# Kernel tuning notes

Hardware: AMD Instinct MI355X
Metric: run time of the kernel (lower is better)

The kernel has to match this reference:

```python
import jax, jax.numpy as jnp
import numpy as np

B = 32; H = 56; W = 56; C = 192; WS = 7; SHIFT = 3; NH = 6
HD = C // NH; N = WS * WS; MLP = 4 * C; NWH = H // WS; NWW = W // WS
EPS = 1e-5


def _rel_pos_index():
    coords = np.stack(np.meshgrid(np.arange(WS), np.arange(WS), indexing='ij'))  # (2,WS,WS)
    cf = coords.reshape(2, -1)                      # (2, N)
    rel = (cf[:, :, None] - cf[:, None, :]).transpose(1, 2, 0).astype(np.int64)  # (N,N,2)
    rel[..., 0] += WS - 1
    rel[..., 1] += WS - 1
    rel[..., 0] *= 2 * WS - 1
    return jnp.asarray(rel.sum(-1))                 # (N, N) int

REL_IDX = _rel_pos_index()


def _shift_mask():
    img = np.zeros((1, H, W, 1), np.float32)
    cnt = 0
    for hs in (slice(0, -WS), slice(-WS, -SHIFT), slice(-SHIFT, None)):
        for ws_ in (slice(0, -WS), slice(-WS, -SHIFT), slice(-SHIFT, None)):
            img[:, hs, ws_, :] = cnt
            cnt += 1
    mw = img.reshape(1, NWH, WS, NWW, WS, 1).transpose(0, 1, 3, 2, 4, 5).reshape(-1, N)
    am = mw[:, None, :] - mw[:, :, None]
    return jnp.asarray(np.where(am != 0, -100.0, 0.0).astype(np.float32))  # (nW, N, N)


def setup_inputs() -> dict:
    key = jax.random.key(0)
    ks = jax.random.split(key, 8)
    s = 0.02
    return {
        'x': jax.random.normal(ks[0], (B, H * W, C), jnp.float32),
        'attn_mask': _shift_mask(),
        'norm1_w': jnp.ones((C,), jnp.float32),
        'norm1_b': jnp.zeros((C,), jnp.float32),
        'qkv_w': jax.random.normal(ks[1], (3 * C, C), jnp.float32) * s,
        'qkv_b': jnp.zeros((3 * C,), jnp.float32),
        'rpb_table': jax.random.normal(ks[2], ((2 * WS - 1) ** 2, NH), jnp.float32) * s,
        'proj_w': jax.random.normal(ks[3], (C, C), jnp.float32) * s,
        'proj_b': jnp.zeros((C,), jnp.float32),
        'norm2_w': jnp.ones((C,), jnp.float32),
        'norm2_b': jnp.zeros((C,), jnp.float32),
        'fc1_w': jax.random.normal(ks[4], (MLP, C), jnp.float32) * s,
        'fc1_b': jnp.zeros((MLP,), jnp.float32),
        'fc2_w': jax.random.normal(ks[5], (C, MLP), jnp.float32) * s,
        'fc2_b': jnp.zeros((C,), jnp.float32),
    }


def _ln(x, w, b):
    m = jnp.mean(x, axis=-1, keepdims=True)
    v = jnp.mean(jnp.square(x - m), axis=-1, keepdims=True)
    return (x - m) * jax.lax.rsqrt(v + EPS) * w + b


def reference(x, attn_mask, norm1_w, norm1_b, qkv_w, qkv_b, rpb_table,
              proj_w, proj_b, norm2_w, norm2_b, fc1_w, fc1_b, fc2_w, fc2_b):
    shortcut = x
    xs = _ln(x, norm1_w, norm1_b).reshape(B, H, W, C)
    # cyclic shift
    xs = jnp.roll(xs, (-SHIFT, -SHIFT), axis=(1, 2))
    # window partition -> (B*nW, N, C)
    xw = xs.reshape(B, NWH, WS, NWW, WS, C).transpose(0, 1, 3, 2, 4, 5).reshape(-1, N, C)
    B_ = xw.shape[0]
    # qkv
    qkv = xw @ qkv_w.T + qkv_b                       # (B_, N, 3C)
    qkv = qkv.reshape(B_, N, 3, NH, HD).transpose(2, 0, 3, 1, 4)
    q, k, v = qkv[0], qkv[1], qkv[2]                 # (B_, NH, N, HD)
    scale = HD ** -0.5
    attn = jnp.einsum('bhnd,bhmd->bhnm', q * scale, k)
    # relative position bias: (N,N,NH) -> (NH,N,N)
    bias = rpb_table[REL_IDX.reshape(-1)].reshape(N, N, NH).transpose(2, 0, 1)
    attn = attn + bias[None]
    # shift mask: (nW, N, N)
    nW = attn_mask.shape[0]
    attn = attn.reshape(B_ // nW, nW, NH, N, N) + attn_mask[None, :, None]
    attn = jax.nn.softmax(attn.reshape(B_, NH, N, N), axis=-1)
    out = jnp.einsum('bhnm,bhmd->bhnd', attn, v)     # (B_, NH, N, HD)
    out = out.transpose(0, 2, 1, 3).reshape(B_, N, C)
    out = out @ proj_w.T + proj_b
    # window reverse -> (B, H, W, C)
    xr = out.reshape(B, NWH, NWW, WS, WS, C).transpose(0, 1, 3, 2, 4, 5).reshape(B, H, W, C)
    xr = jnp.roll(xr, (SHIFT, SHIFT), axis=(1, 2)).reshape(B, H * W, C)
    x = shortcut + xr
    # MLP
    h = _ln(x, norm2_w, norm2_b)
    h = jax.nn.gelu(h @ fc1_w.T + fc1_b, approximate=False)
    h = h @ fc2_w.T + fc2_b
    return x + h
```

## Files before the change

### kernel.cpp

```cpp
#include <hip/hip_runtime.h>
#include <hip/hip_bf16.h>

typedef unsigned short u16;
typedef __attribute__((ext_vector_type(8))) short bf16x8;
typedef __attribute__((ext_vector_type(4))) float f32x4;

#define MFMA16(a, b, c) __builtin_amdgcn_mfma_f32_16x16x32_bf16(a, b, c, 0, 0, 0)

__device__ __forceinline__ u16 f2b(float f) {
  union { float f; unsigned u; } x; x.f = f;
  return (u16)((x.u + 0x7fffu + ((x.u >> 16) & 1u)) >> 16);
}

__device__ __forceinline__ void gload_lds16(const void* g, void* l) {
  __builtin_amdgcn_global_load_lds(
      (const __attribute__((address_space(1))) void*)g,
      (__attribute__((address_space(3))) void*)l, 16, 0, 0);
}

template <int NCH>
__device__ __forceinline__ void stage_frags(const u16* __restrict__ src,
                                            u16* dst, int wave, int lane) {
#pragma unroll
  for (int it = 0; it < NCH / 4; ++it) {
    int chunk = it * 4 + wave;
    gload_lds16(src + ((size_t)chunk * 64 + lane) * 8, dst + chunk * 512);
  }
}

__global__ __launch_bounds__(256) void pack_kernel(const float* __restrict__ W,
                                                   u16* __restrict__ F, int NT,
                                                   int KS, int K, int kmajor) {
  int f = blockIdx.x * 256 + threadIdx.x;
  if (f >= NT * KS * 64) return;
  int l = f & 63, rest = f >> 6;
  int ks, ct;
  if (kmajor) { ct = rest % NT; ks = rest / NT; }
  else        { ks = rest % KS; ct = rest / KS; }
  int row = ct * 16 + (l & 15);
  int col = ks * 32 + (l >> 4) * 8;
  const float* s = W + (size_t)row * K + col;
  u16* d = F + (size_t)f * 8;
#pragma unroll
  for (int i = 0; i < 8; ++i) d[i] = f2b(s[i]);
}

__global__ __launch_bounds__(256) void pack2_kernel(const float* __restrict__ W,
                                                    u16* __restrict__ F) {
  int f = blockIdx.x * 256 + threadIdx.x;
  if (f >= 24 * 12 * 64) return;
  int l = f & 63, rest = f >> 6;
  int ct = rest % 12, hs = rest / 12;
  int row = ct * 16 + (l & 15);
  int g = l >> 4;
  u16* d = F + (size_t)f * 8;
#pragma unroll
  for (int i = 0; i < 8; ++i) {
    int h = hs * 32 + (i < 4 ? 4 * g + i : 16 + 4 * g + (i - 4));
    d[i] = f2b(W[(size_t)row * 768 + h]);
  }
}

__global__ __launch_bounds__(256) void pack_proj_pi(const float* __restrict__ W,
                                                    u16* __restrict__ F) {
  int f = blockIdx.x * 256 + threadIdx.x;
  if (f >= 72 * 64) return;
  int l = f & 63, rest = f >> 6;
  int half = rest / 36, r2 = rest - half * 36;
  int ks = r2 / 6, ctl = r2 - ks * 6;
  int row = (half * 6 + ctl) * 16 + (l & 15);
  int g = l >> 4;
  u16* d = F + (size_t)f * 8;
#pragma unroll
  for (int i = 0; i < 8; ++i) {
    int k = ks * 32 + (i < 4 ? 4 * g + i : 16 + 4 * g + (i - 4));
    d[i] = f2b(W[(size_t)row * 192 + k]);
  }
}

__global__ __launch_bounds__(256, 3) void attn_win(
    const float* __restrict__ x, const float* __restrict__ n1w,
    const float* __restrict__ n1b, const u16* __restrict__ qkvwf,
    const float* __restrict__ qkvb_, const float* __restrict__ rpb,
    const float* __restrict__ amask, const u16* __restrict__ pwf,
    const float* __restrict__ pb, float* __restrict__ out) {
  __shared__ __align__(16) u16 lds[25088];
  u16* wbuf = lds;
  u16* sA   = lds;
  u16* klds = lds + 18432;
  u16* vlds = lds + 21000;
  int tid = threadIdx.x, wave = tid >> 6, lane = tid & 63;
  int g = lane >> 4, c = lane & 15, wr = wave * 16;
  int wing = blockIdx.x;
  int wi = wing & 63;
  {
    float vals[12][4];
    int srcrow[4];
#pragma unroll
    for (int reg = 0; reg < 4; ++reg) {
      int n = wr + 4 * g + reg;
      if (n > 48) n = 48;
      int bb = wing >> 6, wloc = wing & 63, wh = wloc >> 3, ww = wloc & 7;
      int rr = n / 7, cc = n - rr * 7;
      int hs = wh * 7 + rr + 3; if (hs >= 56) hs -= 56;
      int wsr = ww * 7 + cc + 3; if (wsr >= 56) wsr -= 56;
      srcrow[reg] = bb * 3136 + hs * 56 + wsr;
    }
#pragma unroll
    for (int nt = 0; nt < 12; ++nt)
#pragma unroll
      for (int reg = 0; reg < 4; ++reg)
        vals[nt][reg] = x[(size_t)srcrow[reg] * 192 + nt * 16 + c];
#pragma unroll
    for (int reg = 0; reg < 4; ++reg) {
      float s = 0.f;
#pragma unroll
      for (int nt = 0; nt < 12; ++nt) s += vals[nt][reg];
      s += __shfl_xor(s, 1, 64); s += __shfl_xor(s, 2, 64);
      s += __shfl_xor(s, 4, 64); s += __shfl_xor(s, 8, 64);
      float m = s * (1.f / 192.f), q = 0.f;
#pragma unroll
      for (int nt = 0; nt < 12; ++nt) { float d = vals[nt][reg] - m; q += d * d; }
      q += __shfl_xor(q, 1, 64); q += __shfl_xor(q, 2, 64);
      q += __shfl_xor(q, 4, 64); q += __shfl_xor(q, 8, 64);
      float rs = rsqrtf(q * (1.f / 192.f) + 1e-5f);
#pragma unroll
      for (int nt = 0; nt < 12; ++nt) vals[nt][reg] = (vals[nt][reg] - m) * rs;
    }
#pragma unroll
    for (int nt = 0; nt < 12; ++nt) {
      float wv = n1w[nt * 16 + c], bv = n1b[nt * 16 + c];
#pragma unroll
      for (int reg = 0; reg < 4; ++reg) {
        int r = wr + 4 * g + reg;
        int ch = nt * 2 + (c >> 3);
        int ph = (ch & 24) | ((ch ^ (r & 7)) & 7);
        sA[r * 192 + ph * 8 + (c & 7)] = f2b(vals[nt][reg] * wv + bv);
      }
    }
  }
  __syncthreads();
  bf16x8 afr[6];
  {
    int ar = wr + c;
#pragma unroll
    for (int ks = 0; ks < 6; ++ks) {
      int ch = ks * 4 + g;
      int ph = (ch & 24) | ((ch ^ (ar & 7)) & 7);
      afr[ks] = *(const bf16x8*)(sA + ar * 192 + ph * 8);
    }
  }
  __syncthreads();
#pragma unroll
  for (int s = 0; s < 3; ++s)
    stage_frags<12>(qkvwf + (size_t)((s * 12 + 0) * 6) * 512, wbuf + s * 6144,
                    wave, lane);
  int nq = wr + c;
  int nb = nq > 48 ? 48 : nq;
  int ridx[16];
  float pm[16];
  {
    int i1 = nb / 7, j1 = nb - i1 * 7;
#pragma unroll
    for (int kt = 0; kt < 4; ++kt)
#pragma unroll
      for (int reg = 0; reg < 4; ++reg) {
        int m = kt * 16 + 4 * g + reg;
        int idx = kt * 4 + reg;
        if (m < 49) {
          int i2 = m / 7, j2 = m - i2 * 7;
          ridx[idx] = ((i1 - i2 + 6) * 13 + (j1 - j2 + 6)) * 6;
          pm[idx] = amask[(size_t)wi * 2401 + nb * 49 + m];
        } else {
          ridx[idx] = 0;
          pm[idx] = -1e30f;
        }
      }
  }
  __syncthreads();
  bf16x8 ofr[6];
#pragma unroll
  for (int h = 0; h < 6; ++h) {
    f32x4 qa[2], ka[2], va[2];
#pragma unroll
    for (int s = 0; s < 3; ++s)
#pragma unroll
      for (int t = 0; t < 2; ++t) {
        f32x4 acc = {0.f, 0.f, 0.f, 0.f};
#pragma unroll
        for (int ks = 0; ks < 6; ++ks) {
          bf16x8 wf = *(const bf16x8*)(wbuf + (s * 12 + t * 6 + ks) * 512 +
                                       lane * 8);
          acc = MFMA16(wf, afr[ks], acc);
        }
        float4 b4 = *(const float4*)(qkvb_ + s * 192 + h * 32 + t * 16 + 4 * g);
#pragma unroll
        for (int reg = 0; reg < 4; ++reg) acc[reg] += ((const float*)&b4)[reg];
        if (s == 0) qa[t] = acc;
        else if (s == 1) ka[t] = acc;
        else va[t] = acc;
      }
    union { u16 hh[8]; bf16x8 v; } qf, kf;
#pragma unroll
    for (int reg = 0; reg < 4; ++reg) {
      qf.hh[reg] = f2b(qa[0][reg]);
      qf.hh[reg + 4] = f2b(qa[1][reg]);
      kf.hh[reg] = f2b(ka[0][reg]);
      kf.hh[reg + 4] = f2b(ka[1][reg]);
    }
    *(bf16x8*)(klds + nq * 40 + g * 8) = kf.v;
#pragma unroll
    for (int t = 0; t < 2; ++t)
#pragma unroll
      for (int reg = 0; reg < 4; ++reg)
        vlds[(t * 16 + 4 * g + reg) * 68 + nq] = f2b(va[t][reg]);
    __syncthreads();
    if (h < 5) {
#pragma unroll
      for (int s = 0; s < 3; ++s)
        stage_frags<12>(qkvwf + (size_t)((s * 12 + (h + 1) * 2) * 6) * 512,
                        wbuf + s * 6144, wave, lane);
    }
    float sv[16];
#pragma unroll
    for (int kt = 0; kt < 4; ++kt) {
      bf16x8 kw = *(const bf16x8*)(klds + (kt * 16 + c) * 40 + g * 8);
      f32x4 z = {0.f, 0.f, 0.f, 0.f};
      f32x4 sacc = MFMA16(kw, qf.v, z);
#pragma unroll
      for (int reg = 0; reg < 4; ++reg) sv[kt * 4 + reg] = sacc[reg];
    }
    const float scale = 0.17677669529663687f;
    float mx = -1e30f;
#pragma unroll
    for (int i = 0; i < 16; ++i) {
      sv[i] = sv[i] * scale + rpb[ridx[i] + h] + pm[i];
      mx = fmaxf(mx, sv[i]);
    }
    mx = fmaxf(mx, __shfl_xor(mx, 16, 64));
    mx = fmaxf(mx, __shfl_xor(mx, 32, 64));
    float se = 0.f;
#pragma unroll
    for (int i = 0; i < 16; ++i) {
      sv[i] = __expf(sv[i] - mx);
      se += sv[i];
    }
    se += __shfl_xor(se, 16, 64);
    se += __shfl_xor(se, 32, 64);
    float inv = 1.0f / se;
    union { u16 hh[8]; bf16x8 v; } pu0, pu1;
#pragma unroll
    for (int reg = 0; reg < 4; ++reg) {
      pu0.hh[reg] = f2b(sv[0 * 4 + reg] * inv);
      pu0.hh[reg + 4] = f2b(sv[1 * 4 + reg] * inv);
      pu1.hh[reg] = f2b(sv[2 * 4 + reg] * inv);
      pu1.hh[reg + 4] = f2b(sv[3 * 4 + reg] * inv);
    }
    f32x4 oacc[2] = {{0, 0, 0, 0}, {0, 0, 0, 0}};
#pragma unroll
    for (int nt = 0; nt < 2; ++nt)
#pragma unroll
      for (int mblk = 0; mblk < 2; ++mblk) {
        const u16* vp = vlds + (nt * 16 + c) * 68 + mblk * 32 + 4 * g;
        union { u16 hh[8]; bf16x8 v; } vt;
        *(short4*)(vt.hh) = *(const short4*)(vp);
        *(short4*)(vt.hh + 4) = *(const short4*)(vp + 16);
        oacc[nt] = MFMA16(vt.v, mblk ? pu1.v : pu0.v, oacc[nt]);
      }
    {
      union { u16 hh[8]; bf16x8 v; } of_;
#pragma unroll
      for (int reg = 0; reg < 4; ++reg) {
        of_.hh[reg] = f2b(oacc[0][reg]);
        of_.hh[reg + 4] = f2b(oacc[1][reg]);
      }
      ofr[h] = of_.v;
    }
    __syncthreads();
  }
  size_t trow = 0;
  if (nq < 49) {
    int rr = nq / 7, cc2 = nq - rr * 7;
    int wloc = wing & 63, wh = wloc >> 3, ww2 = wloc & 7;
    int hs2 = wh * 7 + rr + 3; if (hs2 >= 56) hs2 -= 56;
    int ws2 = ww2 * 7 + cc2 + 3; if (ws2 >= 56) ws2 -= 56;
    trow = (size_t)(wing >> 6) * 3136 + hs2 * 56 + ws2;
  }
#pragma unroll
  for (int half = 0; half < 2; ++half) {
#pragma unroll
    for (int it = 0; it < 9; ++it) {
      int chunk = it * 4 + wave;
      gload_lds16(pwf + ((size_t)(half * 36 + chunk) * 64 + lane) * 8,
                  lds + chunk * 512);
    }
    asm volatile("s_waitcnt vmcnt(0)" ::: "memory");
    __syncthreads();
    f32x4 op6[6];
#pragma unroll
    for (int i = 0; i < 6; ++i) op6[i] = (f32x4){0.f, 0.f, 0.f, 0.f};
#pragma unroll
    for (int ks = 0; ks < 6; ++ks)
#pragma unroll
      for (int ctl = 0; ctl < 6; ++ctl) {
        bf16x8 wf = *(const bf16x8*)(lds + (ks * 6 + ctl) * 512 + lane * 8);
        op6[ctl] = MFMA16(wf, ofr[ks], op6[ctl]);
      }
    if (nq < 49) {
      float* rowp = out + trow * 192 + half * 96;
      const float* xp = x + trow * 192 + half * 96;
#pragma unroll
      for (int ctl = 0; ctl < 6; ++ctl) {
        int colo = ctl * 16 + 4 * g;
        float4 xv = *(const float4*)(xp + colo);
        float4 b4 = *(const float4*)(pb + half * 96 + colo);
        float4 st;
        st.x = xv.x + op6[ctl][0] + b4.x;
        st.y = xv.y + op6[ctl][1] + b4.y;
        st.z = xv.z + op6[ctl][2] + b4.z;
        st.w = xv.w + op6[ctl][3] + b4.w;
        *(float4*)(rowp + colo) = st;
      }
    }
    __syncthreads();
  }
}

__global__ __launch_bounds__(256, 3) void mlp_fused(
    const float* __restrict__ n2w, const float* __restrict__ n2b,
    const u16* __restrict__ w1f, const float* __restrict__ b1,
    const u16* __restrict__ w2f, const float* __restrict__ b2,
    float* __restrict__ out) {
  __shared__ __align__(16) u16 lds[24576];
  u16* c1a = lds;
  u16* c1b = lds + 6144;
  u16* c2a = lds + 12288;
  u16* c2b = lds + 18432;
  u16* sA  = lds;
  int tid = threadIdx.x, wave = tid >> 6, lane = tid & 63;
  int g = lane >> 4, c = lane & 15, wr = wave * 16;
  int m0 = blockIdx.x * 64;
  {
    float v[12][4];
    int rr[4];
#pragma unroll
    for (int reg = 0; reg < 4; ++reg) rr[reg] = m0 + wr + 4 * g + reg;
#pragma unroll
    for (int nt = 0; nt < 12; ++nt)
#pragma unroll
      for (int reg = 0; reg < 4; ++reg)
        v[nt][reg] = out[(size_t)rr[reg] * 192 + nt * 16 + c];
#pragma unroll
    for (int reg = 0; reg < 4; ++reg) {
      float s = 0.f;
#pragma unroll
      for (int nt = 0; nt < 12; ++nt) s += v[nt][reg];
      s += __shfl_xor(s, 1, 64); s += __shfl_xor(s, 2, 64);
      s += __shfl_xor(s, 4, 64); s += __shfl_xor(s, 8, 64);
      float m = s * (1.f / 192.f), q = 0.f;
#pragma unroll
      for (int nt = 0; nt < 12; ++nt) { float d = v[nt][reg] - m; q += d * d; }
      q += __shfl_xor(q, 1, 64); q += __shfl_xor(q, 2, 64);
      q += __shfl_xor(q, 4, 64); q += __shfl_xor(q, 8, 64);
      float rs = rsqrtf(q * (1.f / 192.f) + 1e-5f);
#pragma unroll
      for (int nt = 0; nt < 12; ++nt) v[nt][reg] = (v[nt][reg] - m) * rs;
    }
#pragma unroll
    for (int nt = 0; nt < 12; ++nt) {
      float wv = n2w[nt * 16 + c], bv = n2b[nt * 16 + c];
#pragma unroll
      for (int reg = 0; reg < 4; ++reg) {
        int r = wr + 4 * g + reg;
        int ch = nt * 2 + (c >> 3);
        int ph = (ch & 24) | ((ch ^ (r & 7)) & 7);
        sA[r * 192 + ph * 8 + (c & 7)] = f2b(v[nt][reg] * wv + bv);
      }
    }
  }
  __syncthreads();
  bf16x8 afr[6];
  {
    int ar = wr + c;
#pragma unroll
    for (int ks = 0; ks < 6; ++ks) {
      int ch = ks * 4 + g;
      int ph = (ch & 24) | ((ch ^ (ar & 7)) & 7);
      afr[ks] = *(const bf16x8*)(sA + ar * 192 + ph * 8);
    }
  }
  __syncthreads();
  stage_frags<12>(w1f, c1a, wave, lane);
  stage_frags<12>(w2f, c2a, wave, lane);
  f32x4 o[12];
#pragma unroll
  for (int i = 0; i < 12; ++i) o[i] = (f32x4){0.f, 0.f, 0.f, 0.f};
  __syncthreads();
  for (int j = 0; j < 24; ++j) {
    int cur = j & 1;
    const u16* r1 = cur ? c1b : c1a;
    const u16* r2 = cur ? c2b : c2a;
    if (j < 23) {
      stage_frags<12>(w1f + (size_t)(j + 1) * 6144, cur ? c1a : c1b, wave, lane);
      stage_frags<12>(w2f + (size_t)(j + 1) * 6144, cur ? c2a : c2b, wave, lane);
    }
    f32x4 S1[2] = {{0,0,0,0},{0,0,0,0}};
#pragma unroll
    for (int ks = 0; ks < 6; ++ks) {
      bf16x8 w0 = *(const bf16x8*)(r1 + (0 * 6 + ks) * 512 + lane * 8);
      bf16x8 w1v = *(const bf16x8*)(r1 + (1 * 6 + ks) * 512 + lane * 8);
      S1[0] = MFMA16(w0, afr[ks], S1[0]);
      S1[1] = MFMA16(w1v, afr[ks], S1[1]);
    }
    union { u16 h[8]; bf16x8 v; } pu;
    float4 bv0 = *(const float4*)(b1 + j * 32 + 4 * g);
    float4 bv1 = *(const float4*)(b1 + j * 32 + 16 + 4 * g);
#pragma unroll
    for (int r = 0; r < 4; ++r) {
      float v0 = S1[0][r] + ((const float*)&bv0)[r];
      float u20 = v0 * (1.5957691216f + 0.0713548163f * v0 * v0);
      pu.h[r] = f2b(v0 / (1.f + __expf(-u20)));
      float v1 = S1[1][r] + ((const float*)&bv1)[r];
      float u21 = v1 * (1.5957691216f + 0.0713548163f * v1 * v1);
      pu.h[r + 4] = f2b(v1 / (1.f + __expf(-u21)));
    }
#pragma unroll
    for (int ct = 0; ct < 12; ++ct) {
      bf16x8 wf2 = *(const bf16x8*)(r2 + ct * 512 + lane * 8);
      o[ct] = MFMA16(wf2, pu.v, o[ct]);
    }
    __syncthreads();
  }
  size_t rowoff = (size_t)(m0 + wr + c) * 192;
#pragma unroll
  for (int ct = 0; ct < 12; ++ct) {
    float4 b4 = *(const float4*)(b2 + ct * 16 + 4 * g);
#pragma unroll
    for (int r = 0; r < 4; ++r) {
      size_t oo = rowoff + ct * 16 + 4 * g + r;
      out[oo] = out[oo] + o[ct][r] + ((const float*)&b4)[r];
    }
  }
}

extern "C" void kernel_launch(void* const* d_in, const int* in_sizes, int n_in,
                              void* d_out, int out_size, void* d_ws, size_t ws_size,
                              hipStream_t stream) {
  (void)in_sizes; (void)n_in; (void)out_size; (void)ws_size;
  const float* x     = (const float*)d_in[0];
  const float* amask = (const float*)d_in[1];
  const float* n1w   = (const float*)d_in[2];
  const float* n1b   = (const float*)d_in[3];
  const float* qkvw  = (const float*)d_in[4];
  const float* qkvb  = (const float*)d_in[5];
  const float* rpb   = (const float*)d_in[6];
  const float* projw = (const float*)d_in[7];
  const float* projb = (const float*)d_in[8];
  const float* n2w   = (const float*)d_in[9];
  const float* n2b   = (const float*)d_in[10];
  const float* fc1w  = (const float*)d_in[11];
  const float* fc1b  = (const float*)d_in[12];
  const float* fc2w  = (const float*)d_in[13];
  const float* fc2b  = (const float*)d_in[14];
  float* out = (float*)d_out;
  char* ws = (char*)d_ws;

  u16* qkvwf = (u16*)(ws);
  u16* projwf = (u16*)(ws + 221184);
  u16* fc1wf = (u16*)(ws + 221184 + 73728);
  u16* fc2wf = (u16*)(ws + 221184 + 73728 + 294912);

  pack_kernel<<<(36 * 6 * 64 + 255) / 256, 256, 0, stream>>>(qkvw, qkvwf, 36, 6, 192, 0);
  pack_proj_pi<<<(72 * 64 + 255) / 256, 256, 0, stream>>>(projw, projwf);
  pack_kernel<<<(48 * 6 * 64 + 255) / 256, 256, 0, stream>>>(fc1w, fc1wf, 48, 6, 192, 0);
  pack2_kernel<<<(24 * 12 * 64 + 255) / 256, 256, 0, stream>>>(fc2w, fc2wf);

  attn_win<<<2048, 256, 0, stream>>>(x, n1w, n1b, qkvwf, qkvb, rpb, amask,
                                     projwf, projb, out);

  mlp_fused<<<1568, 256, 0, stream>>>(n2w, n2b, fc1wf, fc1b, fc2wf, fc2b,
                                      out);
}
```

Measured before the change: 254.5 us.

## Single-buffer MLP weights for higher occupancy, prefetch proj weights, use native bf16 cvt

The MLP kernel drops double-buffered weight staging, which halves its LDS and raises launch bounds to 6 blocks per CU, but each step now waits synchronously for the next weight load. The attention kernel starts loading the first half of the projection weights during the last head iteration and trims its LDS allocation. Manual bf16 rounding is replaced with the HIP intrinsic conversion, and divisions become hardware reciprocals. Together these aim to raise occupancy and cut ALU work, at the cost of losing load/compute overlap in the MLP loop.

Result: slower. 449.4 us (+76.6%).

```diff
diff --git a/kernel.cpp b/kernel.cpp
--- a/kernel.cpp
+++ b/kernel.cpp
@@ -10,6 +10,12 @@
 __device__ __forceinline__ u16 f2b(float f) {
   union { float f; unsigned u; } x; x.f = f;
   return (u16)((x.u + 0x7fffu + ((x.u >> 16) & 1u)) >> 16);
+}
+
+__device__ __forceinline__ u16 f2bn(float f) {
+  union { __hip_bfloat16 b; u16 u; } cv;
+  cv.b = __float2bfloat16(f);
+  return cv.u;
 }
 
 __device__ __forceinline__ void gload_lds16(const void* g, void* l) {
@@ -84,7 +90,7 @@
     const float* __restrict__ qkvb_, const float* __restrict__ rpb,
     const float* __restrict__ amask, const u16* __restrict__ pwf,
     const float* __restrict__ pb, float* __restrict__ out) {
-  __shared__ __align__(16) u16 lds[25088];
+  __shared__ __align__(16) u16 lds[23176];
   u16* wbuf = lds;
   u16* sA   = lds;
   u16* klds = lds + 18432;
@@ -135,7 +141,7 @@
         int r = wr + 4 * g + reg;
         int ch = nt * 2 + (c >> 3);
         int ph = (ch & 24) | ((ch ^ (r & 7)) & 7);
-        sA[r * 192 + ph * 8 + (c & 7)] = f2b(vals[nt][reg] * wv + bv);
+        sA[r * 192 + ph * 8 + (c & 7)] = f2bn(vals[nt][reg] * wv + bv);
       }
     }
   }
@@ -203,23 +209,25 @@
     union { u16 hh[8]; bf16x8 v; } qf, kf;
 #pragma unroll
     for (int reg = 0; reg < 4; ++reg) {
-      qf.hh[reg] = f2b(qa[0][reg]);
-      qf.hh[reg + 4] = f2b(qa[1][reg]);
-      kf.hh[reg] = f2b(ka[0][reg]);
-      kf.hh[reg + 4] = f2b(ka[1][reg]);
+      qf.hh[reg] = f2bn(qa[0][reg]);
+      qf.hh[reg + 4] = f2bn(qa[1][reg]);
+      kf.hh[reg] = f2bn(ka[0][reg]);
+      kf.hh[reg + 4] = f2bn(ka[1][reg]);
     }
     *(bf16x8*)(klds + nq * 40 + g * 8) = kf.v;
 #pragma unroll
     for (int t = 0; t < 2; ++t)
 #pragma unroll
       for (int reg = 0; reg < 4; ++reg)
-        vlds[(t * 16 + 4 * g + reg) * 68 + nq] = f2b(va[t][reg]);
+        vlds[(t * 16 + 4 * g + reg) * 68 + nq] = f2bn(va[t][reg]);
     __syncthreads();
     if (h < 5) {
 #pragma unroll
       for (int s = 0; s < 3; ++s)
         stage_frags<12>(qkvwf + (size_t)((s * 12 + (h + 1) * 2) * 6) * 512,
                         wbuf + s * 6144, wave, lane);
+    } else {
+      stage_frags<36>(pwf, wbuf, wave, lane);
     }
     float sv[16];
 #pragma unroll
@@ -247,14 +255,14 @@
     }
     se += __shfl_xor(se, 16, 64);
     se += __shfl_xor(se, 32, 64);
-    float inv = 1.0f / se;
+    float inv = __builtin_amdgcn_rcpf(se);
     union { u16 hh[8]; bf16x8 v; } pu0, pu1;
 #pragma unroll
     for (int reg = 0; reg < 4; ++reg) {
-      pu0.hh[reg] = f2b(sv[0 * 4 + reg] * inv);
-      pu0.hh[reg + 4] = f2b(sv[1 * 4 + reg] * inv);
-      pu1.hh[reg] = f2b(sv[2 * 4 + reg] * inv);
-      pu1.hh[reg + 4] = f2b(sv[3 * 4 + reg] * inv);
+      pu0.hh[reg] = f2bn(sv[0 * 4 + reg] * inv);
+      pu0.hh[reg + 4] = f2bn(sv[1 * 4 + reg] * inv);
+      pu1.hh[reg] = f2bn(sv[2 * 4 + reg] * inv);
+      pu1.hh[reg + 4] = f2bn(sv[3 * 4 + reg] * inv);
     }
     f32x4 oacc[2] = {{0, 0, 0, 0}, {0, 0, 0, 0}};
 #pragma unroll
@@ -271,8 +279,8 @@
       union { u16 hh[8]; bf16x8 v; } of_;
 #pragma unroll
       for (int reg = 0; reg < 4; ++reg) {
-        of_.hh[reg] = f2b(oacc[0][reg]);
-        of_.hh[reg + 4] = f2b(oacc[1][reg]);
+        of_.hh[reg] = f2bn(oacc[0][reg]);
+        of_.hh[reg + 4] = f2bn(oacc[1][reg]);
       }
       ofr[h] = of_.v;
     }
@@ -288,14 +296,6 @@
   }
 #pragma unroll
   for (int half = 0; half < 2; ++half) {
-#pragma unroll
-    for (int it = 0; it < 9; ++it) {
-      int chunk = it * 4 + wave;
-      gload_lds16(pwf + ((size_t)(half * 36 + chunk) * 64 + lane) * 8,
-                  lds + chunk * 512);
-    }
-    asm volatile("s_waitcnt vmcnt(0)" ::: "memory");
-    __syncthreads();
     f32x4 op6[6];
 #pragma unroll
     for (int i = 0; i < 6; ++i) op6[i] = (f32x4){0.f, 0.f, 0.f, 0.f};
@@ -322,21 +322,23 @@
         *(float4*)(rowp + colo) = st;
       }
     }
-    __syncthreads();
-  }
-}
-
-__global__ __launch_bounds__(256, 3) void mlp_fused(
+    if (half == 0) {
+      __syncthreads();
+      stage_frags<36>(pwf + (size_t)36 * 512, lds, wave, lane);
+      __syncthreads();
+    }
+  }
+}
+
+__global__ __launch_bounds__(256, 6) void mlp_fused(
     const float* __restrict__ n2w, const float* __restrict__ n2b,
     const u16* __restrict__ w1f, const float* __restrict__ b1,
     const u16* __restrict__ w2f, const float* __restrict__ b2,
     float* __restrict__ out) {
-  __shared__ __align__(16) u16 lds[24576];
-  u16* c1a = lds;
-  u16* c1b = lds + 6144;
-  u16* c2a = lds + 12288;
-  u16* c2b = lds + 18432;
-  u16* sA  = lds;
+  __shared__ __align__(16) u16 lds[12288];
+  u16* c1 = lds;
+  u16* c2 = lds + 6144;
+  u16* sA = lds;
   int tid = threadIdx.x, wave = tid >> 6, lane = tid & 63;
   int g = lane >> 4, c = lane & 15, wr = wave * 16;
   int m0 = blockIdx.x * 64;
@@ -374,7 +376,7 @@
         int r = wr + 4 * g + reg;
         int ch = nt * 2 + (c >> 3);
         int ph = (ch & 24) | ((ch ^ (r & 7)) & 7);
-        sA[r * 192 + ph * 8 + (c & 7)] = f2b(v[nt][reg] * wv + bv);
+        sA[r * 192 + ph * 8 + (c & 7)] = f2bn(v[nt][reg] * wv + bv);
       }
     }
   }
@@ -390,25 +392,18 @@
     }
   }
   __syncthreads();
-  stage_frags<12>(w1f, c1a, wave, lane);
-  stage_frags<12>(w2f, c2a, wave, lane);
+  stage_frags<12>(w1f, c1, wave, lane);
+  stage_frags<12>(w2f, c2, wave, lane);
   f32x4 o[12];
 #pragma unroll
   for (int i = 0; i < 12; ++i) o[i] = (f32x4){0.f, 0.f, 0.f, 0.f};
   __syncthreads();
   for (int j = 0; j < 24; ++j) {
-    int cur = j & 1;
-    const u16* r1 = cur ? c1b : c1a;
-    const u16* r2 = cur ? c2b : c2a;
-    if (j < 23) {
-      stage_frags<12>(w1f + (size_t)(j + 1) * 6144, cur ? c1a : c1b, wave, lane);
-      stage_frags<12>(w2f + (size_t)(j + 1) * 6144, cur ? c2a : c2b, wave, lane);
-    }
     f32x4 S1[2] = {{0,0,0,0},{0,0,0,0}};
 #pragma unroll
     for (int ks = 0; ks < 6; ++ks) {
-      bf16x8 w0 = *(const bf16x8*)(r1 + (0 * 6 + ks) * 512 + lane * 8);
-      bf16x8 w1v = *(const bf16x8*)(r1 + (1 * 6 + ks) * 512 + lane * 8);
+      bf16x8 w0 = *(const bf16x8*)(c1 + (0 * 6 + ks) * 512 + lane * 8);
+      bf16x8 w1v = *(const bf16x8*)(c1 + (1 * 6 + ks) * 512 + lane * 8);
       S1[0] = MFMA16(w0, afr[ks], S1[0]);
       S1[1] = MFMA16(w1v, afr[ks], S1[1]);
     }
@@ -419,17 +414,22 @@
     for (int r = 0; r < 4; ++r) {
       float v0 = S1[0][r] + ((const float*)&bv0)[r];
       float u20 = v0 * (1.5957691216f + 0.0713548163f * v0 * v0);
-      pu.h[r] = f2b(v0 / (1.f + __expf(-u20)));
+      pu.h[r] = f2bn(v0 * __builtin_amdgcn_rcpf(1.f + __expf(-u20)));
       float v1 = S1[1][r] + ((const float*)&bv1)[r];
       float u21 = v1 * (1.5957691216f + 0.0713548163f * v1 * v1);
-      pu.h[r + 4] = f2b(v1 / (1.f + __expf(-u21)));
+      pu.h[r + 4] = f2bn(v1 * __builtin_amdgcn_rcpf(1.f + __expf(-u21)));
     }
 #pragma unroll
     for (int ct = 0; ct < 12; ++ct) {
-      bf16x8 wf2 = *(const bf16x8*)(r2 + ct * 512 + lane * 8);
+      bf16x8 wf2 = *(const bf16x8*)(c2 + ct * 512 + lane * 8);
       o[ct] = MFMA16(wf2, pu.v, o[ct]);
     }
     __syncthreads();
+    if (j < 23) {
+      stage_frags<12>(w1f + (size_t)(j + 1) * 6144, c1, wave, lane);
+      stage_frags<12>(w2f + (size_t)(j + 1) * 6144, c2, wave, lane);
+      __syncthreads();
+    }
   }
   size_t rowoff = (size_t)(m0 + wr + c) * 192;
 #pragma unroll
```
